# Optimization experiments

Hardware: AMD Instinct MI355X
Metric: run time of the kernel (lower is better)

Reference implementation:

```python
import jax, jax.numpy as jnp
import numpy as np


def setup_inputs() -> dict:
    key = jax.random.key(0)
    k1, k2 = jax.random.split(key)
    B, L, D = 2, 512, 256  # D = 2*hidden_size, Linear in-dim = 2*D = 512
    inputs = jax.random.normal(k1, (B, L, D), dtype=jnp.float32)
    W = jax.random.normal(k2, (2 * D, 1), dtype=jnp.float32) * 0.02
    b = jnp.zeros((1,), dtype=jnp.float32)
    return {"inputs": inputs, "W": W, "b": b}


def reference(inputs, W, b):
    # Original: prod = x_i * x_j, diff = x_i - x_j, cat -> Linear(4H, 1), symmetrize.
    # Dropout is identity in eval mode.
    # Algebraically identical split of the Linear: W = [w1; w2] over (prod, diff):
    #   pred_ij = sum_d x_id x_jd w1_d + sum_d (x_id - x_jd) w2_d + b
    D = inputs.shape[-1]
    w1 = W[:D, 0]   # [D] weights over prod features
    w2 = W[D:, 0]   # [D] weights over diff features
    # bilinear term via small GEMM: (x * w1) @ x^T  -> [B, L, L]
    bilin = jnp.einsum('bid,bjd->bij', inputs * w1, inputs)
    lin = inputs @ w2  # [B, L]
    pred = bilin + lin[:, :, None] - lin[:, None, :] + b[0]  # [B, L, L]
    pred = pred[..., None]  # [B, L, L, 1] matching Linear(...,1) output
    pred = (pred + jnp.swapaxes(pred, 1, 2)) * 0.5
    return (pred,)
```

## Files before the change

### kernel.cpp

```cpp
#include <hip/hip_runtime.h>
#include <hip/hip_bf16.h>


constexpr int Lc = 512;
constexpr int Dc = 256;

typedef __attribute__((ext_vector_type(8))) short short8;
typedef __attribute__((ext_vector_type(4))) float f32x4;

__device__ __forceinline__ short f2bf(float f) {
    __hip_bfloat16 h = __float2bfloat16(f);
    return __builtin_bit_cast(short, h);
}

__global__ __launch_bounds__(64)
void pairwise_mfma_kernel(const float* __restrict__ x,
                          const float* __restrict__ W,
                          const float* __restrict__ bvec,
                          float* __restrict__ out)
{
    const int lane = threadIdx.x;
    const int j0 = blockIdx.x * 16;
    const int i0 = blockIdx.y * 16;
    const int b  = blockIdx.z;

    const int lm = lane & 15;
    const int kh = lane >> 4;

    const float* xa = x + (size_t)b * Lc * Dc + (size_t)(i0 + lm) * Dc + 8 * kh;
    const float* xb = x + (size_t)b * Lc * Dc + (size_t)(j0 + lm) * Dc + 8 * kh;
    const float* wp = W + 8 * kh;

    f32x4 acc = {0.f, 0.f, 0.f, 0.f};

#pragma unroll
    for (int ks = 0; ks < Dc; ks += 32) {
        const float4 a0 = *(const float4*)(xa + ks);
        const float4 a1 = *(const float4*)(xa + ks + 4);
        const float4 b0 = *(const float4*)(xb + ks);
        const float4 b1 = *(const float4*)(xb + ks + 4);
        const float4 w0 = *(const float4*)(wp + ks);
        const float4 w1 = *(const float4*)(wp + ks + 4);

        short8 af, bf;
        af[0] = f2bf(a0.x * w0.x);  af[1] = f2bf(a0.y * w0.y);
        af[2] = f2bf(a0.z * w0.z);  af[3] = f2bf(a0.w * w0.w);
        af[4] = f2bf(a1.x * w1.x);  af[5] = f2bf(a1.y * w1.y);
        af[6] = f2bf(a1.z * w1.z);  af[7] = f2bf(a1.w * w1.w);
        bf[0] = f2bf(b0.x);         bf[1] = f2bf(b0.y);
        bf[2] = f2bf(b0.z);         bf[3] = f2bf(b0.w);
        bf[4] = f2bf(b1.x);         bf[5] = f2bf(b1.y);
        bf[6] = f2bf(b1.z);         bf[7] = f2bf(b1.w);

        acc = __builtin_amdgcn_mfma_f32_16x16x32_bf16(af, bf, acc, 0, 0, 0);
    }

    const float bb = bvec[0];
    float* op = out + ((size_t)b * Lc + (i0 + 4 * kh)) * Lc + (j0 + lm);
#pragma unroll
    for (int r = 0; r < 4; ++r)
        op[(size_t)r * Lc] = acc[r] + bb;
}

extern "C" void kernel_launch(void* const* d_in, const int* in_sizes, int n_in,
                              void* d_out, int out_size, void* d_ws, size_t ws_size,
                              hipStream_t stream) {
    const float* x    = (const float*)d_in[0];
    const float* W    = (const float*)d_in[1];
    const float* bias = (const float*)d_in[2];
    float* out        = (float*)d_out;

    dim3 grid(Lc / 16, Lc / 16, 2);
    dim3 block(64);
    pairwise_mfma_kernel<<<grid, block, 0, stream>>>(x, W, bias, out);
}
```

Measured before the change: 65.85 us.

## Pre-convert inputs to bf16 workspace and compute 32x32 tiles per wave

Adds a separate conversion kernel that scales x by w1 and writes bf16 copies of both operands into the workspace once. The Gram kernel then loads bf16 directly instead of reconverting fp32 data for every tile. Each wave now computes a 32x32 output tile with four MFMAs, so each loaded fragment is reused twice. The cost is an extra kernel launch, a workspace round trip, and fewer blocks in the grid.

```diff
diff --git a/kernel.cpp b/kernel.cpp
--- a/kernel.cpp
+++ b/kernel.cpp
@@ -13,53 +13,75 @@
     return __builtin_bit_cast(short, h);
 }
 
+__global__ __launch_bounds__(256)
+void convert_kernel(const float* __restrict__ x, const float* __restrict__ W,
+                    short* __restrict__ aws, short* __restrict__ bws)
+{
+    const int base = (blockIdx.x * 256 + threadIdx.x) * 8;
+    const int d = base & (Dc - 1);
+
+    const float4 x0 = *(const float4*)(x + base);
+    const float4 x1 = *(const float4*)(x + base + 4);
+    const float4 w0 = *(const float4*)(W + d);
+    const float4 w1 = *(const float4*)(W + d + 4);
+
+    short8 a, b;
+    a[0] = f2bf(x0.x * w0.x); a[1] = f2bf(x0.y * w0.y);
+    a[2] = f2bf(x0.z * w0.z); a[3] = f2bf(x0.w * w0.w);
+    a[4] = f2bf(x1.x * w1.x); a[5] = f2bf(x1.y * w1.y);
+    a[6] = f2bf(x1.z * w1.z); a[7] = f2bf(x1.w * w1.w);
+    b[0] = f2bf(x0.x); b[1] = f2bf(x0.y); b[2] = f2bf(x0.z); b[3] = f2bf(x0.w);
+    b[4] = f2bf(x1.x); b[5] = f2bf(x1.y); b[6] = f2bf(x1.z); b[7] = f2bf(x1.w);
+
+    *(short8*)(aws + base) = a;
+    *(short8*)(bws + base) = b;
+}
+
 __global__ __launch_bounds__(64)
-void pairwise_mfma_kernel(const float* __restrict__ x,
-                          const float* __restrict__ W,
-                          const float* __restrict__ bvec,
-                          float* __restrict__ out)
+void gram_mfma_kernel(const short* __restrict__ aws,
+                      const short* __restrict__ bws,
+                      const float* __restrict__ bvec,
+                      float* __restrict__ out)
 {
     const int lane = threadIdx.x;
-    const int j0 = blockIdx.x * 16;
-    const int i0 = blockIdx.y * 16;
+    const int j0 = blockIdx.x * 32;
+    const int i0 = blockIdx.y * 32;
     const int b  = blockIdx.z;
 
     const int lm = lane & 15;
     const int kh = lane >> 4;
 
-    const float* xa = x + (size_t)b * Lc * Dc + (size_t)(i0 + lm) * Dc + 8 * kh;
-    const float* xb = x + (size_t)b * Lc * Dc + (size_t)(j0 + lm) * Dc + 8 * kh;
-    const float* wp = W + 8 * kh;
+    const size_t xoff = (size_t)b * Lc * Dc;
+    const short* ap0 = aws + xoff + (size_t)(i0 + lm)      * Dc + 8 * kh;
+    const short* ap1 = aws + xoff + (size_t)(i0 + 16 + lm) * Dc + 8 * kh;
+    const short* bp0 = bws + xoff + (size_t)(j0 + lm)      * Dc + 8 * kh;
+    const short* bp1 = bws + xoff + (size_t)(j0 + 16 + lm) * Dc + 8 * kh;
 
-    f32x4 acc = {0.f, 0.f, 0.f, 0.f};
+    f32x4 acc00 = {0,0,0,0}, acc01 = {0,0,0,0};
+    f32x4 acc10 = {0,0,0,0}, acc11 = {0,0,0,0};
 
 #pragma unroll
     for (int ks = 0; ks < Dc; ks += 32) {
-        const float4 a0 = *(const float4*)(xa + ks);
-        const float4 a1 = *(const float4*)(xa + ks + 4);
-        const float4 b0 = *(const float4*)(xb + ks);
-        const float4 b1 = *(const float4*)(xb + ks + 4);
-        const float4 w0 = *(const float4*)(wp + ks);
-        const float4 w1 = *(const float4*)(wp + ks + 4);
-
-        short8 af, bf;
-        af[0] = f2bf(a0.x * w0.x);  af[1] = f2bf(a0.y * w0.y);
-        af[2] = f2bf(a0.z * w0.z);  af[3] = f2bf(a0.w * w0.w);
-        af[4] = f2bf(a1.x * w1.x);  af[5] = f2bf(a1.y * w1.y);
-        af[6] = f2bf(a1.z * w1.z);  af[7] = f2bf(a1.w * w1.w);
-        bf[0] = f2bf(b0.x);         bf[1] = f2bf(b0.y);
-        bf[2] = f2bf(b0.z);         bf[3] = f2bf(b0.w);
-        bf[4] = f2bf(b1.x);         bf[5] = f2bf(b1.y);
-        bf[6] = f2bf(b1.z);         bf[7] = f2bf(b1.w);
-
-        acc = __builtin_amdgcn_mfma_f32_16x16x32_bf16(af, bf, acc, 0, 0, 0);
+        const short8 a0 = *(const short8*)(ap0 + ks);
+        const short8 a1 = *(const short8*)(ap1 + ks);
+        const short8 b0 = *(const short8*)(bp0 + ks);
+        const short8 b1 = *(const short8*)(bp1 + ks);
+        acc00 = __builtin_amdgcn_mfma_f32_16x16x32_bf16(a0, b0, acc00, 0, 0, 0);
+        acc01 = __builtin_amdgcn_mfma_f32_16x16x32_bf16(a0, b1, acc01, 0, 0, 0);
+        acc10 = __builtin_amdgcn_mfma_f32_16x16x32_bf16(a1, b0, acc10, 0, 0, 0);
+        acc11 = __builtin_amdgcn_mfma_f32_16x16x32_bf16(a1, b1, acc11, 0, 0, 0);
     }
 
     const float bb = bvec[0];
-    float* op = out + ((size_t)b * Lc + (i0 + 4 * kh)) * Lc + (j0 + lm);
+    const size_t obase = (size_t)b * Lc * Lc;
 #pragma unroll
-    for (int r = 0; r < 4; ++r)
-        op[(size_t)r * Lc] = acc[r] + bb;
+    for (int r = 0; r < 4; ++r) {
+        const size_t row0 = i0 + 4 * kh + r;
+        out[obase + row0 * Lc + (j0 + lm)]             = acc00[r] + bb;
+        out[obase + row0 * Lc + (j0 + 16 + lm)]        = acc01[r] + bb;
+        out[obase + (row0 + 16) * Lc + (j0 + lm)]      = acc10[r] + bb;
+        out[obase + (row0 + 16) * Lc + (j0 + 16 + lm)] = acc11[r] + bb;
+    }
 }
 
 extern "C" void kernel_launch(void* const* d_in, const int* in_sizes, int n_in,
@@ -70,7 +92,10 @@
     const float* bias = (const float*)d_in[2];
     float* out        = (float*)d_out;
 
-    dim3 grid(Lc / 16, Lc / 16, 2);
-    dim3 block(64);
-    pairwise_mfma_kernel<<<grid, block, 0, stream>>>(x, W, bias, out);
+    short* aws = (short*)d_ws;
+    short* bws = (short*)d_ws + (size_t)2 * Lc * Dc;
+
+    convert_kernel<<<dim3(128), dim3(256), 0, stream>>>(x, W, aws, bws);
+    gram_mfma_kernel<<<dim3(Lc / 32, Lc / 32, 2), dim3(64), 0, stream>>>(
+        aws, bws, bias, out);
 }
```

New measurement: 61.33 us. 1.07x faster.
